# Performance work log

Measured on AMD Instinct MI355X. Metric: run time of the kernel, lower is better.

The kernel has to match this reference:

```python
import jax, jax.numpy as jnp
import numpy as np

NUM_HEADS = 8

def _avg_pool_3x3_s2(x):
    # x: [BN, H, W, C]; AvgPool2d(kernel=3, stride=2, padding=1, count_include_pad=True)
    s = jax.lax.reduce_window(x, 0.0, jax.lax.add, (1, 3, 3, 1), (1, 2, 2, 1),
                              [(0, 0), (1, 1), (1, 1), (0, 0)])
    return s / 9.0

def _rel_dist(q_size, k_size):
    q_ratio = max(k_size / q_size, 1.0)
    k_ratio = max(q_size / k_size, 1.0)
    d = np.arange(q_size)[:, None] * q_ratio - np.arange(k_size)[None, :] * k_ratio
    d += (k_size - 1) * k_ratio
    return jnp.asarray(d.astype(np.int32))

def setup_inputs() -> dict:
    key = jax.random.key(0)
    ks = jax.random.split(key, 8)
    B, C, H, W = 128, 1024, 24, 24
    hd = C // NUM_HEADS
    rel_dim = 2 * max(H // 2, H) - 1  # 47
    return {
        "x": jax.random.normal(ks[0], (B, C, H, W), jnp.float32),
        "Wq": jax.random.normal(ks[1], (C, C), jnp.float32) * 0.02,
        "Wk": jax.random.normal(ks[2], (C, C), jnp.float32) * 0.02,
        "Wv": jax.random.normal(ks[3], (C, C), jnp.float32) * 0.02,
        "Wp": jax.random.normal(ks[4], (C, C), jnp.float32) * 0.02,
        "bp": jnp.zeros((C,), jnp.float32),
        "rel_pos_h": jax.random.normal(ks[5], (rel_dim, hd), jnp.float32) * 0.02,
        "rel_pos_w": jax.random.normal(ks[6], (rel_dim, hd), jnp.float32) * 0.02,
    }

def reference(x, Wq, Wk, Wv, Wp, bp, rel_pos_h, rel_pos_w):
    B, C, H, W = x.shape
    nh = NUM_HEADS
    hd = C // nh
    N = H * W
    xt = x.reshape(B, C, N).transpose(0, 2, 1)            # [B, N, C]
    # pool_first: split into heads, avg-pool Q spatially (K, V unpooled)
    xh = xt.reshape(B, N, nh, hd).transpose(0, 2, 1, 3)   # [B, nh, N, hd]
    qp = _avg_pool_3x3_s2(xh.reshape(B * nh, H, W, hd))   # [B*nh, 12, 12, hd]
    qh, qw = qp.shape[1], qp.shape[2]
    qN = qh * qw
    # merge heads back, apply per-branch linears (no bias)
    q = qp.reshape(B, nh, qN, hd).transpose(0, 2, 1, 3).reshape(B, qN, C) @ Wq
    q = q.reshape(B, qN, nh, hd).transpose(0, 2, 1, 3)    # [B, nh, qN, hd]
    k = (xt @ Wk).reshape(B, N, nh, hd).transpose(0, 2, 1, 3)
    v = (xt @ Wv).reshape(B, N, nh, hd).transpose(0, 2, 1, 3)
    scale = hd ** -0.5
    attn = jnp.einsum('bhqd,bhkd->bhqk', q * scale, k)    # [B, nh, qN, N]
    # spatial relative position bias
    Rh = rel_pos_h[_rel_dist(qh, H)]                      # [qh, H, hd]
    Rw = rel_pos_w[_rel_dist(qw, W)]                      # [qw, W, hd]
    r_q = q.reshape(B, nh, qh, qw, hd)
    rel_h = jnp.einsum('byhwc,hkc->byhwk', r_q, Rh)       # [B, nh, qh, qw, H]
    rel_w = jnp.einsum('byhwc,wkc->byhwk', r_q, Rw)       # [B, nh, qh, qw, W]
    attn = (attn.reshape(B, nh, qh, qw, H, W)
            + rel_h[..., :, None] + rel_w[..., None, :]).reshape(B, nh, qN, N)
    attn = jax.nn.softmax(attn, axis=-1)
    out = jnp.einsum('bhqk,bhkd->bhqd', attn, v) + q      # residual pooling
    out = out.transpose(0, 2, 1, 3).reshape(B, qN, C) @ Wp + bp
    return out.reshape(B, qh, qw, C).transpose(0, 3, 1, 2)  # [B, C, 12, 12]
```

## Files before the change

kernel.cpp:

```cpp
#include <hip/hip_runtime.h>
#include <hip/hip_bf16.h>

using bf16 = __hip_bfloat16;
typedef __attribute__((ext_vector_type(8))) short short8;
typedef __attribute__((ext_vector_type(4))) short s16x4;
typedef __attribute__((ext_vector_type(4))) float f32x4;

#define MFMA(a,b,c) __builtin_amdgcn_mfma_f32_16x16x32_bf16(a, b, c, 0, 0, 0)

#define B_      128
#define C_      1024
#define NH      8
#define HD      128
#define HW      24
#define NTOK    576
#define QH      12
#define QN      144

static __device__ __forceinline__ float bf2f(bf16 v) { return __bfloat162float(v); }
static __device__ __forceinline__ bf16  f2bf(float v) { return __float2bfloat16(v); }
static __device__ __forceinline__ float s2f(short s) {
    return __uint_as_float(((unsigned)(unsigned short)s) << 16);
}
static __device__ __forceinline__ unsigned bfbits(float v) {
    bf16 t = f2bf(v);
    return (unsigned)*(unsigned short*)&t;
}

__device__ __forceinline__ void gll16(const bf16* src, bf16* dst_lds) {
    __builtin_amdgcn_global_load_lds(
        (__attribute__((address_space(1))) const unsigned int*)src,
        (__attribute__((address_space(3))) unsigned int*)dst_lds,
        16, 0, 0);
}

__global__ __launch_bounds__(256) void transpose_x(
    const float* __restrict__ in, bf16* __restrict__ out)
{
    __shared__ float tile[64][65];
    const int b = blockIdx.z;
    const int t0 = blockIdx.x * 64;
    const int c0 = blockIdx.y * 64;
    const int thr = threadIdx.x;
    const int tx = thr & 15, cr = thr >> 4;

    #pragma unroll
    for (int p = 0; p < 4; p++) {
        int c = cr + p * 16;
        float4 v = *(const float4*)(in + ((size_t)b * C_ + c0 + c) * NTOK + t0 + tx * 4);
        tile[c][tx * 4 + 0] = v.x;
        tile[c][tx * 4 + 1] = v.y;
        tile[c][tx * 4 + 2] = v.z;
        tile[c][tx * 4 + 3] = v.w;
    }
    __syncthreads();

    const int wv = thr >> 6, lane = thr & 63;
    const int ccp = (lane & 31) * 2;
    const int trh = lane >> 5;
    #pragma unroll
    for (int i = 0; i < 8; i++) {
        int tr = wv * 16 + trh + i * 2;
        unsigned u = bfbits(tile[ccp][tr]) | (bfbits(tile[ccp + 1][tr]) << 16);
        *(unsigned*)(out + ((size_t)b * NTOK + t0 + tr) * C_ + c0 + ccp) = u;
    }
}

__global__ __launch_bounds__(256) void transpose_w4(
    const float* __restrict__ p0, const float* __restrict__ p1,
    const float* __restrict__ p2, const float* __restrict__ p3,
    bf16* __restrict__ out)
{
    __shared__ float tile[32][33];
    int z = blockIdx.z;
    const float* ib = (z == 0) ? p0 : (z == 1) ? p1 : (z == 2) ? p2 : p3;
    bf16* ob = out + (size_t)z * 1048576;
    int c0 = blockIdx.x * 32, r0 = blockIdx.y * 32;
    int tx = threadIdx.x & 31, ty = threadIdx.x >> 5;
    #pragma unroll
    for (int i = 0; i < 32; i += 8)
        tile[ty + i][tx] = ib[(size_t)(r0 + ty + i) * 1024 + c0 + tx];
    __syncthreads();
    #pragma unroll
    for (int i = 0; i < 32; i += 8)
        ob[(size_t)(c0 + ty + i) * 1024 + r0 + tx] = f2bf(tile[tx][ty + i]);
}

__global__ __launch_bounds__(256) void pool_kernel(const bf16* __restrict__ xt,
                                                   bf16* __restrict__ xp)
{
    int bqn = blockIdx.x;
    int b = bqn / QN, qn = bqn % QN;
    int y = qn / QH, x = qn % QH;
    int t = threadIdx.x;
    float s0 = 0, s1 = 0, s2 = 0, s3 = 0;
    for (int dy = 0; dy < 3; dy++) {
        int hy = 2 * y - 1 + dy;
        if (hy < 0 || hy >= HW) continue;
        for (int dx = 0; dx < 3; dx++) {
            int hx = 2 * x - 1 + dx;
            if (hx < 0 || hx >= HW) continue;
            const bf16* row = xt + (size_t)(b * NTOK + hy * HW + hx) * C_;
            s0 += bf2f(row[t]);
            s1 += bf2f(row[t + 256]);
            s2 += bf2f(row[t + 512]);
            s3 += bf2f(row[t + 768]);
        }
    }
    bf16* o = xp + (size_t)bqn * C_;
    const float n = 1.f / 9.f;
    o[t] = f2bf(s0 * n); o[t + 256] = f2bf(s1 * n);
    o[t + 512] = f2bf(s2 * n); o[t + 768] = f2bf(s3 * n);
}

template<int EPI>
__device__ __forceinline__ void epi_store(void* Cout, int row, int col, float v,
                                          const float* bias) {
    if constexpr (EPI == 0) {
        ((bf16*)Cout)[(size_t)row * C_ + col] = f2bf(v);
    } else if constexpr (EPI == 2) {
        int bb = col / QN, qn = col % QN;
        ((float*)Cout)[(size_t)bb * (C_ * QN) + (size_t)row * QN + qn] = v + bias[row];
    } else if constexpr (EPI == 3) {
        int b = row / NTOK, n = row % NTOK;
        int h = col >> 7, ci = col & 127;
        int kt2 = n >> 5, kf = (n >> 4) & 1, klane = n & 15;
        int ks2 = ci >> 5, chunk = (ci >> 3) & 3, e = ci & 7;
        int lane = chunk * 16 + klane;
        size_t addr = ((((size_t)(b * NH + h) * 18 + kt2) * 2 + kf) * 4 + ks2) * 512
                      + lane * 8 + e;
        ((bf16*)Cout)[addr] = f2bf(v);
    } else {
        int b = col / NTOK, n = col % NTOK;
        int h = row >> 7, ci = row & 127;
        int hf = (ci >> 4) & 7, lanelo = ci & 15;
        int kt2 = n >> 5, chunk = (n >> 3) & 3, e = n & 7;
        int lane = chunk * 16 + lanelo;
        size_t addr = (((size_t)(b * NH + h) * 18 + kt2) * 8 + hf) * 512
                      + lane * 8 + e;
        ((bf16*)Cout)[addr] = f2bf(v);
    }
}

template<int EPI, int GRP>
__global__ __launch_bounds__(256, 2) void gemm_nt(
    const bf16* __restrict__ A, const bf16* __restrict__ Bt,
    void* __restrict__ Cout, const float* __restrict__ bias)
{
    __shared__ bf16 lds[2][2][128 * 64];
    const int tid = threadIdx.x;
    const int wv = tid >> 6, ln = tid & 63;
    const int id = blockIdx.x;
    const int dm = id & 7, mid = (id >> 3) & 7, grp = id >> 6;
    const int mt = (GRP == 1) ? grp * 8 + dm : mid;
    const int nt = (GRP == 1) ? mid : grp * 8 + dm;
    const int m0 = mt * 128, n0 = nt * 128;
    const int wr = wv >> 1, wc = wv & 1;
    const int l15 = ln & 15, l4 = ln >> 4;
    const int r8 = ln >> 3, sl = ln & 7;
    const int sg = sl ^ r8;

    const bf16* gA = A + (size_t)m0 * C_;
    const bf16* gB = Bt + (size_t)n0 * C_;

    f32x4 zero = {0.f, 0.f, 0.f, 0.f};
    f32x4 acc[4][4];
    #pragma unroll
    for (int i = 0; i < 4; i++)
        #pragma unroll
        for (int j = 0; j < 4; j++) acc[i][j] = zero;

    auto stage = [&](int kt, int d) {
        const bf16* sa = gA + kt * 64;
        const bf16* sb = gB + kt * 64;
        bf16* la = lds[d][0];
        bf16* lb = lds[d][1];
        #pragma unroll
        for (int i = 0; i < 4; i++) {
            int chunk = wv * 4 + i;
            gll16(sa + (size_t)(chunk * 8 + r8) * C_ + sg * 8, la + chunk * 512);
            gll16(sb + (size_t)(chunk * 8 + r8) * C_ + sg * 8, lb + chunk * 512);
        }
    };

    stage(0, 0);
    asm volatile("s_waitcnt vmcnt(0)");
    __syncthreads();

    int cur = 0;
    for (int kt = 0; kt < 16; kt++) {
        if (kt < 15) stage(kt + 1, cur ^ 1);
        const bf16* la = lds[cur][0];
        const bf16* lb = lds[cur][1];
        #pragma unroll
        for (int ks = 0; ks < 2; ks++) {
            short8 af[4], bfr[4];
            #pragma unroll
            for (int fm = 0; fm < 4; fm++) {
                int row = wr * 64 + fm * 16 + l15;
                int slot = (ks * 4 + l4) ^ (row & 7);
                af[fm] = *(const short8*)((const char*)la + row * 128 + slot * 16);
            }
            #pragma unroll
            for (int fn = 0; fn < 4; fn++) {
                int row = wc * 64 + fn * 16 + l15;
                int slot = (ks * 4 + l4) ^ (row & 7);
                bfr[fn] = *(const short8*)((const char*)lb + row * 128 + slot * 16);
            }
            #pragma unroll
            for (int fm = 0; fm < 4; fm++)
                #pragma unroll
                for (int fn = 0; fn < 4; fn++)
                    acc[fm][fn] = MFMA(af[fm], bfr[fn], acc[fm][fn]);
        }
        asm volatile("s_waitcnt vmcnt(0)");
        __syncthreads();
        cur ^= 1;
    }

    #pragma unroll
    for (int fm = 0; fm < 4; fm++)
        #pragma unroll
        for (int fn = 0; fn < 4; fn++)
            #pragma unroll
            for (int r = 0; r < 4; r++)
                epi_store<EPI>(Cout, m0 + wr * 64 + fm * 16 + l4 * 4 + r,
                               n0 + wc * 64 + fn * 16 + l15, acc[fm][fn][r], bias);
}

template<int EPI, int GRP>
__global__ __launch_bounds__(512) void gemm256(
    const bf16* __restrict__ A, const bf16* __restrict__ Bt, void* __restrict__ Cout)
{
    __shared__ bf16 lds[2][32768];

    const int tid = threadIdx.x;
    const int wv = tid >> 6, ln = tid & 63;
    const int wm = wv >> 2, wn = wv & 3;
    const int l15 = ln & 15, l4 = ln >> 4;
    const int r8 = ln >> 3, sg = (ln & 7) ^ r8;

    const int id = blockIdx.x;
    const int dm = id & 7, q4 = (id >> 3) & 3, gq = id >> 5;
    const int mt = (GRP == 1) ? gq * 8 + dm : q4;
    const int nt = (GRP == 1) ? q4 : gq * 8 + dm;
    const size_t m0 = (size_t)mt * 256, n0 = (size_t)nt * 256;

    const bf16* gA = A + m0 * C_;
    const bf16* gB = Bt + n0 * C_;

    f32x4 zero = {0.f, 0.f, 0.f, 0.f};
    f32x4 acc[8][4];
    #pragma unroll
    for (int i = 0; i < 8; i++)
        #pragma unroll
        for (int j = 0; j < 4; j++) acc[i][j] = zero;

    auto stage_part = [&](int t, int part) {
        bf16* dst = &lds[t & 1][part * 8192];
        const bf16* src = (part < 2) ? (gA + (size_t)(part * 128) * C_ + t * 64)
                                     : (gB + (size_t)((part - 2) * 128) * C_ + t * 64);
        #pragma unroll
        for (int i = 0; i < 2; i++) {
            int chunk = wv * 2 + i;
            gll16(src + (size_t)(chunk * 8 + r8) * C_ + sg * 8, dst + chunk * 512);
        }
    };

    #pragma unroll
    for (int p = 0; p < 4; p++) stage_part(0, p);
    asm volatile("s_waitcnt vmcnt(0)");
    __syncthreads();

    const int brow0 = (wn & 1) * 64;

    for (int t = 0; t < 16; t++) {
        const char* Abase = (const char*)&lds[t & 1][wm * 8192];
        const char* Bbase = (const char*)&lds[t & 1][16384 + (wn >> 1) * 8192];

        if (t < 15) {
            stage_part(t + 1, 0);
            stage_part(t + 1, 1);
            stage_part(t + 1, 2);
            stage_part(t + 1, 3);
        }

        short8 Bf[4][2];
        #pragma unroll
        for (int fn = 0; fn < 4; fn++)
            #pragma unroll
            for (int ks = 0; ks < 2; ks++) {
                int r = brow0 + fn * 16 + l15;
                int slot = (ks * 4 + l4) ^ (r & 7);
                Bf[fn][ks] = *(const short8*)(Bbase + r * 128 + slot * 16);
            }

        {
            short8 Af[4][2];
            #pragma unroll
            for (int fm = 0; fm < 4; fm++)
                #pragma unroll
                for (int ks = 0; ks < 2; ks++) {
                    int r = fm * 16 + l15;
                    int slot = (ks * 4 + l4) ^ (r & 7);
                    Af[fm][ks] = *(const short8*)(Abase + r * 128 + slot * 16);
                }
            __builtin_amdgcn_s_setprio(1);
            #pragma unroll
            for (int fm = 0; fm < 4; fm++)
                #pragma unroll
                for (int fn = 0; fn < 4; fn++)
                    #pragma unroll
                    for (int ks = 0; ks < 2; ks++)
                        acc[fm][fn] = MFMA(Af[fm][ks], Bf[fn][ks], acc[fm][fn]);
            __builtin_amdgcn_s_setprio(0);
        }
        {
            short8 Af[4][2];
            #pragma unroll
            for (int fm = 0; fm < 4; fm++)
                #pragma unroll
                for (int ks = 0; ks < 2; ks++) {
                    int r = (fm + 4) * 16 + l15;
                    int slot = (ks * 4 + l4) ^ (r & 7);
                    Af[fm][ks] = *(const short8*)(Abase + r * 128 + slot * 16);
                }
            __builtin_amdgcn_s_setprio(1);
            #pragma unroll
            for (int fm = 0; fm < 4; fm++)
                #pragma unroll
                for (int fn = 0; fn < 4; fn++)
                    #pragma unroll
                    for (int ks = 0; ks < 2; ks++)
                        acc[fm + 4][fn] = MFMA(Af[fm][ks], Bf[fn][ks], acc[fm + 4][fn]);
            __builtin_amdgcn_s_setprio(0);
        }

        asm volatile("s_waitcnt vmcnt(0)");
        __syncthreads();
    }

    #pragma unroll
    for (int fm = 0; fm < 8; fm++)
        #pragma unroll
        for (int fn = 0; fn < 4; fn++)
            #pragma unroll
            for (int r = 0; r < 4; r++)
                epi_store<EPI>(Cout, (int)m0 + wm * 128 + fm * 16 + l4 * 4 + r,
                               (int)n0 + wn * 64 + fn * 16 + l15, acc[fm][fn][r], nullptr);
}

__global__ __launch_bounds__(256) void relcvt_kernel(
    const float* __restrict__ rph, const float* __restrict__ rpw,
    bf16* __restrict__ relph, bf16* __restrict__ relpw)
{
    int i = blockIdx.x * 256 + threadIdx.x;
    if (i < 6144) {
        bool v = i < 6016;
        relph[i] = v ? f2bf(rph[i]) : f2bf(0.f);
        relpw[i] = v ? f2bf(rpw[i]) : f2bf(0.f);
    }
}

__global__ __launch_bounds__(192) void relgemm_kernel(
    const bf16* __restrict__ qbuf, const bf16* __restrict__ relph,
    const bf16* __restrict__ relpw, bf16* __restrict__ rgh, bf16* __restrict__ rgw)
{
    const int bid = blockIdx.x;
    const int bh = bid / 3, qb = bid - bh * 3;
    const int b = bh >> 3, h = bh & 7;
    const int w = threadIdx.x >> 6, ln = threadIdx.x & 63;
    const int l15 = ln & 15, l4 = ln >> 4;
    const int qrow = qb * 48 + w * 16 + l15;
    const int y = qrow / 12, x = qrow - y * 12;

    short8 qfr[4];
    #pragma unroll
    for (int ks = 0; ks < 4; ks++)
        qfr[ks] = *(const short8*)(qbuf + (size_t)(b * QN + qrow) * C_ + h * HD +
                                   ks * 32 + l4 * 8);

    f32x4 zero = {0.f, 0.f, 0.f, 0.f};
    bf16* oh = rgh + (size_t)bh * (QN * 24);
    bf16* ow = rgw + (size_t)bh * (QN * 24);

    #pragma unroll
    for (int tile = 0; tile < 3; tile++) {
        short8 rfh[4], rfw[4];
        #pragma unroll
        for (int ks = 0; ks < 4; ks++) {
            rfh[ks] = *(const short8*)(relph + (tile * 16 + l15) * 128 + ks * 32 + l4 * 8);
            rfw[ks] = *(const short8*)(relpw + (tile * 16 + l15) * 128 + ks * 32 + l4 * 8);
        }
        f32x4 ah = zero, aw = zero;
        #pragma unroll
        for (int ks = 0; ks < 4; ks++) ah = MFMA(rfh[ks], qfr[ks], ah);
        #pragma unroll
        for (int ks = 0; ks < 4; ks++) aw = MFMA(rfw[ks], qfr[ks], aw);
        #pragma unroll
        for (int r = 0; r < 4; r++) {
            int d = tile * 16 + l4 * 4 + r;
            int kr = 2 * y + 23 - d;
            if (kr >= 0 && kr < 24) oh[qrow * 24 + kr] = f2bf(ah[r]);
            int kc = 2 * x + 23 - d;
            if (kc >= 0 && kc < 24) ow[qrow * 24 + kc] = f2bf(aw[r]);
        }
    }
}

__global__ __launch_bounds__(192) void attn_fused(
    const bf16* __restrict__ qbuf, const bf16* __restrict__ kfr,
    const bf16* __restrict__ vfr, const bf16* __restrict__ rgh,
    const bf16* __restrict__ rgw, bf16* __restrict__ attno)
{
    __shared__ bf16 relhL[QN * 24];
    __shared__ bf16 relwL[QN * 24];
    __shared__ bf16 kvlds[2][8192];
    __shared__ char plds[3][1024];

    const int bid = blockIdx.x;
    const int bh = ((bid & 7) * 128) + (bid >> 3);
    const int b = bh >> 3, h = bh & 7;
    const int w = threadIdx.x >> 6, ln = threadIdx.x & 63;
    const int l15 = ln & 15, l4 = ln >> 4;

    const bf16* kh = kfr + (size_t)bh * 18 * 4096;
    const bf16* vh = vfr + (size_t)bh * 18 * 4096;
    const bf16* qhb = qbuf + ((size_t)(b * QN) * C_ + h * HD);

    auto stage = [&](int kt, int d) {
        for (int c = w; c < 16; c += 3) {
            const bf16* src = (c < 8) ? (kh + (size_t)kt * 4096 + c * 512)
                                      : (vh + (size_t)kt * 4096 + (c - 8) * 512);
            gll16(src + ln * 8, &kvlds[d][c * 512]);
        }
    };

    stage(0, 0);

    {
        const short8* gh = (const short8*)(rgh + (size_t)bh * (QN * 24));
        const short8* gw = (const short8*)(rgw + (size_t)bh * (QN * 24));
        for (int i = threadIdx.x; i < 432; i += 192) {
            ((short8*)relhL)[i] = gh[i];
            ((short8*)relwL)[i] = gw[i];
        }
    }

    short8 qfr[3][4];
    #pragma unroll
    for (int s = 0; s < 3; s++)
        #pragma unroll
        for (int ks = 0; ks < 4; ks++)
            qfr[s][ks] = *(const short8*)(qhb + (size_t)(w * 48 + s * 16 + l15) * C_ +
                                          ks * 32 + l4 * 8);

    f32x4 zero = {0.f, 0.f, 0.f, 0.f};
    f32x4 Of[3][8];
    float ls[3] = {0.f, 0.f, 0.f};
    #pragma unroll
    for (int s = 0; s < 3; s++)
        #pragma unroll
        for (int hf = 0; hf < 8; hf++) Of[s][hf] = zero;

    const float scale = 0.08838834764831845f;
    const int xsw = (l15 >> 1) & 3;

    asm volatile("s_waitcnt vmcnt(0)");
    __syncthreads();

    int cur = 0;
    for (int kt = 0; kt < 18; kt++) {
        if (kt < 17) stage(kt + 1, cur ^ 1);
        const bf16* kbuf = &kvlds[cur][0];
        const bf16* vbuf = &kvlds[cur][4096];
        #pragma unroll
        for (int s = 0; s < 3; s++) {
            const int rb = (w * 48 + s * 16 + l15) * 24;
            f32x4 S[2];
            #pragma unroll
            for (int kf = 0; kf < 2; kf++) {
                f32x4 acc = zero;
                #pragma unroll
                for (int ks = 0; ks < 4; ks++) {
                    short8 kb = *(const short8*)(kbuf + (kf * 4 + ks) * 512 + ln * 8);
                    acc = MFMA(kb, qfr[s][ks], acc);
                }
                S[kf] = acc;
            }
            float p[8];
            #pragma unroll
            for (int kf = 0; kf < 2; kf++) {
                #pragma unroll
                for (int r = 0; r < 4; r++) {
                    int key = kt * 32 + kf * 16 + l4 * 4 + r;
                    int kr = key / 24, kc = key - kr * 24;
                    p[kf * 4 + r] = __expf(S[kf][r] * scale + bf2f(relhL[rb + kr]) +
                                           bf2f(relwL[rb + kc]));
                }
            }
            ls[s] += ((p[0] + p[1]) + (p[2] + p[3])) + ((p[4] + p[5]) + (p[6] + p[7]));
            #pragma unroll
            for (int kf = 0; kf < 2; kf++) {
                unsigned u0 = bfbits(p[kf * 4 + 0]) | (bfbits(p[kf * 4 + 1]) << 16);
                unsigned u1 = bfbits(p[kf * 4 + 2]) | (bfbits(p[kf * 4 + 3]) << 16);
                int s16 = (kf * 2 + (l4 >> 1)) ^ xsw;
                *(unsigned long long*)(&plds[w][l15 * 64 + s16 * 16 + (l4 & 1) * 8]) =
                    ((unsigned long long)u1 << 32) | u0;
            }
            short8 pf = *(const short8*)(&plds[w][l15 * 64 + (l4 ^ xsw) * 16]);
            #pragma unroll
            for (int hf = 0; hf < 8; hf++) {
                short8 vb = *(const short8*)(vbuf + hf * 512 + ln * 8);
                Of[s][hf] = MFMA(vb, pf, Of[s][hf]);
            }
        }
        asm volatile("s_waitcnt vmcnt(0)");
        __syncthreads();
        cur ^= 1;
    }

    #pragma unroll
    for (int s = 0; s < 3; s++) {
        float t = ls[s];
        t += __shfl_xor(t, 16, 64);
        t += __shfl_xor(t, 32, 64);
        float inv = 1.f / t;
        int qrow = w * 48 + s * 16 + l15;
        const bf16* qrb = qhb + (size_t)qrow * C_;
        bf16* orb = attno + ((size_t)(b * QN + qrow) * C_ + h * HD);
        #pragma unroll
        for (int hf = 0; hf < 8; hf++) {
            s16x4 qres = *(const s16x4*)(qrb + hf * 16 + l4 * 4);
            s16x4 o;
            #pragma unroll
            for (int r = 0; r < 4; r++) {
                float v = Of[s][hf][r] * inv + s2f(qres[r]);
                o[r] = (short)bfbits(v);
            }
            *(s16x4*)(orb + hf * 16 + l4 * 4) = o;
        }
    }
}

extern "C" void kernel_launch(void* const* d_in, const int* in_sizes, int n_in,
                              void* d_out, int out_size, void* d_ws, size_t ws_size,
                              hipStream_t stream)
{
    const float* x   = (const float*)d_in[0];
    const float* Wq  = (const float*)d_in[1];
    const float* Wk  = (const float*)d_in[2];
    const float* Wv  = (const float*)d_in[3];
    const float* Wp  = (const float*)d_in[4];
    const float* bp  = (const float*)d_in[5];
    const float* rph = (const float*)d_in[6];
    const float* rpw = (const float*)d_in[7];

    char* ws = (char*)d_ws;
    const size_t MB = 1024 * 1024;
    bf16* Wqt  = (bf16*)(ws + 0 * MB);
    bf16* Wkt  = (bf16*)(ws + 2 * MB);
    bf16* Wvt  = (bf16*)(ws + 4 * MB);
    bf16* Wpt  = (bf16*)(ws + 6 * MB);
    bf16* xt   = (bf16*)(ws + 8 * MB);
    bf16* rgh  = (bf16*)(ws + 8 * MB);
    bf16* rgw  = (bf16*)(ws + 16 * MB);
    bf16* relph = (bf16*)(ws + 24 * MB);
    bf16* relpw = (bf16*)(ws + 25 * MB);
    bf16* kfrb = (bf16*)(ws + 152 * MB);
    bf16* vfrb = (bf16*)(ws + 296 * MB);
    bf16* xp   = (bf16*)(ws + 440 * MB);
    bf16* qbuf = (bf16*)(ws + 476 * MB);
    bf16* attno = xp;

    transpose_w4<<<dim3(32, 32, 4), 256, 0, stream>>>(Wq, Wk, Wv, Wp, (bf16*)ws);
    transpose_x<<<dim3(9, 16, 128), 256, 0, stream>>>(x, xt);
    pool_kernel<<<dim3(B_ * QN), 256, 0, stream>>>(xt, xp);
    gemm256<3, 1><<<dim3(1152), 512, 0, stream>>>(xt, Wkt, kfrb);
    gemm256<4, 2><<<dim3(1152), 512, 0, stream>>>(Wvt, xt, vfrb);
    gemm_nt<0, 1><<<dim3(1152), 256, 0, stream>>>(xp, Wqt, qbuf, nullptr);
    relcvt_kernel<<<dim3(24), 256, 0, stream>>>(rph, rpw, relph, relpw);
    relgemm_kernel<<<dim3(B_ * NH * 3), 192, 0, stream>>>(qbuf, relph, relpw, rgh, rgw);
    attn_fused<<<dim3(B_ * NH), 192, 0, stream>>>(qbuf, kfrb, vfrb, rgh, rgw, attno);
    gemm_nt<2, 2><<<dim3(1152), 256, 0, stream>>>(Wpt, attno, d_out, bp);
}
```

Before: 783.4 us.

## Deepen gemm256 pipeline to four-stage ring with K=32 tiles

Replaces the two-buffer K=64 staging in the 256x256 GEMM with a four-slot ring of K=32 tiles, prefetching three tiles ahead. Partial vmcnt waits replace the full drain each iteration, so global loads stay in flight across several compute steps. LDS footprint is unchanged, but there are twice as many iterations and barriers, each with half the MFMA work per step. The swizzled layout is re-derived for the narrower tiles.

```diff
diff --git a/kernel.cpp b/kernel.cpp
--- a/kernel.cpp
+++ b/kernel.cpp
@@ -232,7 +232,7 @@
 __global__ __launch_bounds__(512) void gemm256(
     const bf16* __restrict__ A, const bf16* __restrict__ Bt, void* __restrict__ Cout)
 {
-    __shared__ bf16 lds[2][32768];
+    __shared__ bf16 lds[4][16384];
 
     const int tid = threadIdx.x;
     const int wv = tid >> 6, ln = tid & 63;
@@ -256,88 +256,75 @@
         #pragma unroll
         for (int j = 0; j < 4; j++) acc[i][j] = zero;
 
-    auto stage_part = [&](int t, int part) {
-        bf16* dst = &lds[t & 1][part * 8192];
-        const bf16* src = (part < 2) ? (gA + (size_t)(part * 128) * C_ + t * 64)
-                                     : (gB + (size_t)((part - 2) * 128) * C_ + t * 64);
-        #pragma unroll
-        for (int i = 0; i < 2; i++) {
-            int chunk = wv * 2 + i;
-            gll16(src + (size_t)(chunk * 8 + r8) * C_ + sg * 8, dst + chunk * 512);
+    auto stage = [&](int t) {
+        bf16* buf = lds[t & 3];
+        #pragma unroll
+        for (int i = 0; i < 4; i++) {
+            int c32 = wv * 4 + i;
+            bool isA = c32 < 16;
+            int c = isA ? c32 : c32 - 16;
+            const bf16* g = isA ? gA : gB;
+            int row = (c * 8 + r8) * 2 + (sg >> 2);
+            const bf16* src = g + (size_t)row * C_ + t * 32 + (sg & 3) * 8;
+            gll16(src, buf + (isA ? 0 : 8192) + c * 512 + ln * 8);
         }
     };
 
-    #pragma unroll
-    for (int p = 0; p < 4; p++) stage_part(0, p);
-    asm volatile("s_waitcnt vmcnt(0)");
-    __syncthreads();
+    stage(0); stage(1); stage(2);
 
     const int brow0 = (wn & 1) * 64;
 
-    for (int t = 0; t < 16; t++) {
-        const char* Abase = (const char*)&lds[t & 1][wm * 8192];
-        const char* Bbase = (const char*)&lds[t & 1][16384 + (wn >> 1) * 8192];
-
-        if (t < 15) {
-            stage_part(t + 1, 0);
-            stage_part(t + 1, 1);
-            stage_part(t + 1, 2);
-            stage_part(t + 1, 3);
-        }
-
-        short8 Bf[4][2];
+    for (int t = 0; t < 32; t++) {
+        if (t + 3 < 32) stage(t + 3);
+        if (t < 29)       asm volatile("s_waitcnt vmcnt(12)");
+        else if (t == 29) asm volatile("s_waitcnt vmcnt(8)");
+        else if (t == 30) asm volatile("s_waitcnt vmcnt(4)");
+        else              asm volatile("s_waitcnt vmcnt(0)");
+        __builtin_amdgcn_s_barrier();
+        __builtin_amdgcn_sched_barrier(0);
+
+        const char* Ab = (const char*)lds[t & 3] + wm * 8192;
+        const char* Bb = (const char*)lds[t & 3] + 16384 + (wn >> 1) * 8192;
+        auto fro = [&](int rl) {
+            int pr = rl >> 1;
+            int slv = ((rl & 1) << 2) | l4;
+            return pr * 128 + ((slv ^ (pr & 7)) << 4);
+        };
+
+        short8 Bf[4];
         #pragma unroll
         for (int fn = 0; fn < 4; fn++)
-            #pragma unroll
-            for (int ks = 0; ks < 2; ks++) {
-                int r = brow0 + fn * 16 + l15;
-                int slot = (ks * 4 + l4) ^ (r & 7);
-                Bf[fn][ks] = *(const short8*)(Bbase + r * 128 + slot * 16);
-            }
+            Bf[fn] = *(const short8*)(Bb + fro(brow0 + fn * 16 + l15));
 
         {
-            short8 Af[4][2];
+            short8 Af[4];
             #pragma unroll
             for (int fm = 0; fm < 4; fm++)
-                #pragma unroll
-                for (int ks = 0; ks < 2; ks++) {
-                    int r = fm * 16 + l15;
-                    int slot = (ks * 4 + l4) ^ (r & 7);
-                    Af[fm][ks] = *(const short8*)(Abase + r * 128 + slot * 16);
-                }
+                Af[fm] = *(const short8*)(Ab + fro(fm * 16 + l15));
             __builtin_amdgcn_s_setprio(1);
             #pragma unroll
             for (int fm = 0; fm < 4; fm++)
                 #pragma unroll
                 for (int fn = 0; fn < 4; fn++)
-                    #pragma unroll
-                    for (int ks = 0; ks < 2; ks++)
-                        acc[fm][fn] = MFMA(Af[fm][ks], Bf[fn][ks], acc[fm][fn]);
+                    acc[fm][fn] = MFMA(Af[fm], Bf[fn], acc[fm][fn]);
             __builtin_amdgcn_s_setprio(0);
         }
         {
-            short8 Af[4][2];
+            short8 Af[4];
             #pragma unroll
             for (int fm = 0; fm < 4; fm++)
-                #pragma unroll
-                for (int ks = 0; ks < 2; ks++) {
-                    int r = (fm + 4) * 16 + l15;
-                    int slot = (ks * 4 + l4) ^ (r & 7);
-                    Af[fm][ks] = *(const short8*)(Abase + r * 128 + slot * 16);
-                }
+                Af[fm] = *(const short8*)(Ab + fro((fm + 4) * 16 + l15));
             __builtin_amdgcn_s_setprio(1);
             #pragma unroll
             for (int fm = 0; fm < 4; fm++)
                 #pragma unroll
                 for (int fn = 0; fn < 4; fn++)
-                    #pragma unroll
-                    for (int ks = 0; ks < 2; ks++)
-                        acc[fm + 4][fn] = MFMA(Af[fm][ks], Bf[fn][ks], acc[fm + 4][fn]);
+                    acc[fm + 4][fn] = MFMA(Af[fm], Bf[fn], acc[fm + 4][fn]);
             __builtin_amdgcn_s_setprio(0);
         }
 
-        asm volatile("s_waitcnt vmcnt(0)");
-        __syncthreads();
+        __builtin_amdgcn_s_barrier();
+        __builtin_amdgcn_sched_barrier(0);
     }
 
     #pragma unroll
```

Result: slower. 831.6 us (+6.2%).
